# Kernel optimization log

Hardware: AMD Instinct MI355X
Metric: run time of the kernel (lower is better)

Reference implementation:

```python
import jax, jax.numpy as jnp
import numpy as np

N_NODES = 100000
N_EDGES = 1600000
DIM = 64
LAYERS = 2


def setup_inputs() -> dict:
    key = jax.random.key(0)
    k1, k2, k3, k4 = jax.random.split(key, 4)
    h = jax.random.normal(k1, (N_NODES, DIM), dtype=jnp.float32)
    w = jax.random.uniform(k2, (N_EDGES,), dtype=jnp.float32)
    src = jax.random.randint(k3, (N_EDGES,), 0, N_NODES, dtype=jnp.int32)
    dst = jax.random.randint(k4, (N_EDGES,), 0, N_NODES, dtype=jnp.int32)
    return {"h": h, "w": w, "src": src, "dst": dst}


def reference(h, w, src, dst):
    N = h.shape[0]
    # weighted in-degree, clamped at 1 (DGL in_degrees(weight='w').clamp(min=1))
    deg = jnp.maximum(jax.ops.segment_sum(w, dst, num_segments=N), 1.0)
    norm = deg[:, None] ** -0.5  # [N, 1]
    embs = [h]
    for _ in range(LAYERS):
        h_norm = h * norm                              # [N, d]
        m = h_norm[src] * w[:, None]                   # [E, d] edge messages (u_mul_e)
        neigh_sum = jax.ops.segment_sum(m, dst, num_segments=N)  # fn.sum
        h = neigh_sum * norm
        embs.append(h)
    # mean over [h0, h1, ..., hL]
    return jnp.mean(jnp.stack(embs, axis=1), axis=1)
```

## Files before the change

### kernel.cpp

```cpp
#include <hip/hip_runtime.h>
#include <hip/hip_bf16.h>

#define D 64
#define THREADS 256
#define BKT_BITS 9
#define BKT_NODES (1 << BKT_BITS)
#define CHUNK 8192

__device__ __forceinline__ unsigned f2bf(float f) {
    unsigned u = __float_as_uint(f);
    return (u + 0x7fffu + ((u >> 16) & 1u)) >> 16;
}
__device__ __forceinline__ float2 bfpair(unsigned v) {
    return make_float2(__uint_as_float(v << 16), __uint_as_float(v & 0xffff0000u));
}

typedef unsigned long long u64t;
typedef float f32x4 __attribute__((ext_vector_type(4)));
typedef unsigned u32x4 __attribute__((ext_vector_type(4)));

__device__ __forceinline__ int2 ldnt_int2(const int2* p) {
    u64t v = __builtin_nontemporal_load((const u64t*)p);
    int2 r;
    r.x = (int)(unsigned)(v & 0xffffffffull);
    r.y = (int)(unsigned)(v >> 32);
    return r;
}
__device__ __forceinline__ uint4 ldnt_uint4(const uint4* p) {
    u32x4 v = __builtin_nontemporal_load((const u32x4*)p);
    return make_uint4(v.x, v.y, v.z, v.w);
}
__device__ __forceinline__ void stnt_f4(float4 v, float4* p) {
    f32x4 t = {v.x, v.y, v.z, v.w};
    __builtin_nontemporal_store(t, (f32x4*)p);
}
__device__ __forceinline__ void stnt_u4(uint4 v, uint4* p) {
    u32x4 t = {v.x, v.y, v.z, v.w};
    __builtin_nontemporal_store(t, (u32x4*)p);
}

__global__ void p1a_hist(const int* __restrict__ dst, int* __restrict__ blockCount,
                         int E, int B) {
    __shared__ int lc[256];
    int t = threadIdx.x;
    lc[t] = 0;
    __syncthreads();
    int base = blockIdx.x * CHUNK;
    int end = min(base + CHUNK, E);
    int end4 = end >> 2;
    for (int e4 = (base >> 2) + t; e4 < end4; e4 += THREADS) {
        int4 d4 = ((const int4*)dst)[e4];
        atomicAdd(&lc[d4.x >> BKT_BITS], 1);
        atomicAdd(&lc[d4.y >> BKT_BITS], 1);
        atomicAdd(&lc[d4.z >> BKT_BITS], 1);
        atomicAdd(&lc[d4.w >> BKT_BITS], 1);
    }
    for (int e = (end4 << 2) + t; e < end; e += THREADS)
        atomicAdd(&lc[dst[e] >> BKT_BITS], 1);
    __syncthreads();
    if (t < B) blockCount[(long long)blockIdx.x * B + t] = lc[t];
}

__global__ void p1b_scanblocks(int* __restrict__ blockCount, int* __restrict__ total,
                               int NBLK, int B) {
    __shared__ int sm[256];
    int b = blockIdx.x, t = threadIdx.x;
    int run = 0;
    for (int base = 0; base < NBLK; base += 256) {
        int i = base + t;
        int v = (i < NBLK) ? blockCount[(long long)i * B + b] : 0;
        sm[t] = v;
        __syncthreads();
        for (int off = 1; off < 256; off <<= 1) {
            int u = (t >= off) ? sm[t - off] : 0;
            __syncthreads();
            sm[t] += u;
            __syncthreads();
        }
        if (i < NBLK) blockCount[(long long)i * B + b] = run + sm[t] - v;
        run += sm[255];
        __syncthreads();
    }
    if (t == 0) total[b] = run;
}

__global__ void p1c_scanbuckets(const int* __restrict__ total, int* __restrict__ bstart,
                                int B, int E) {
    __shared__ int sm[256];
    int t = threadIdx.x;
    int run = 0;
    for (int base = 0; base < B; base += 256) {
        int i = base + t;
        int v = (i < B) ? total[i] : 0;
        sm[t] = v;
        __syncthreads();
        for (int off = 1; off < 256; off <<= 1) {
            int u = (t >= off) ? sm[t - off] : 0;
            __syncthreads();
            sm[t] += u;
            __syncthreads();
        }
        if (i < B) bstart[i] = run + sm[t] - v;
        run += sm[255];
        __syncthreads();
    }
    if (t == 0) bstart[B] = E;
}

__global__ void p1d_scatter(const int* __restrict__ dst, const int* __restrict__ src,
                            const float* __restrict__ w, const int* __restrict__ blockCount,
                            const int* __restrict__ bstart, int2* __restrict__ temp,
                            int E, int B) {
    __shared__ int cur[256];
    int t = threadIdx.x;
    if (t < B) cur[t] = bstart[t] + blockCount[(long long)blockIdx.x * B + t];
    __syncthreads();
    int base = blockIdx.x * CHUNK;
    int end = min(base + CHUNK, E);
    int end4 = end >> 2;
    for (int e4 = (base >> 2) + t; e4 < end4; e4 += THREADS) {
        int4 d4 = ((const int4*)dst)[e4];
        int4 s4 = ((const int4*)src)[e4];
        float4 w4 = ((const float4*)w)[e4];
        int pos;
        pos = atomicAdd(&cur[d4.x >> BKT_BITS], 1);
        temp[pos] = make_int2(s4.x | ((d4.x & (BKT_NODES - 1)) << 17), __float_as_int(w4.x));
        pos = atomicAdd(&cur[d4.y >> BKT_BITS], 1);
        temp[pos] = make_int2(s4.y | ((d4.y & (BKT_NODES - 1)) << 17), __float_as_int(w4.y));
        pos = atomicAdd(&cur[d4.z >> BKT_BITS], 1);
        temp[pos] = make_int2(s4.z | ((d4.z & (BKT_NODES - 1)) << 17), __float_as_int(w4.z));
        pos = atomicAdd(&cur[d4.w >> BKT_BITS], 1);
        temp[pos] = make_int2(s4.w | ((d4.w & (BKT_NODES - 1)) << 17), __float_as_int(w4.w));
    }
    for (int e = (end4 << 2) + t; e < end; e += THREADS) {
        int d = dst[e];
        int pos = atomicAdd(&cur[d >> BKT_BITS], 1);
        temp[pos] = make_int2(src[e] | ((d & (BKT_NODES - 1)) << 17), __float_as_int(w[e]));
    }
}

__global__ void p2a_build(const int2* __restrict__ temp, const int* __restrict__ bstart,
                          int* __restrict__ rowptr, float* __restrict__ norm,
                          int N, int E, int B) {
    __shared__ int cnt[BKT_NODES];
    __shared__ float degs[BKT_NODES];
    __shared__ int sm[256];
    int b = blockIdx.x, t = threadIdx.x;
    int ebeg = bstart[b], eend = bstart[b + 1];
    for (int i = t; i < BKT_NODES; i += THREADS) { cnt[i] = 0; degs[i] = 0.0f; }
    __syncthreads();
    for (int e = ebeg + t; e < eend; e += THREADS) {
        int2 pk = temp[e];
        int dl = (pk.x >> 17) & (BKT_NODES - 1);
        atomicAdd(&cnt[dl], 1);
        atomicAdd(&degs[dl], __int_as_float(pk.y));
    }
    __syncthreads();
    int node0 = b << BKT_BITS;
    int run = 0;
    for (int base = 0; base < BKT_NODES; base += 256) {
        int v = cnt[base + t];
        sm[t] = v;
        __syncthreads();
        for (int off = 1; off < 256; off <<= 1) {
            int u = (t >= off) ? sm[t - off] : 0;
            __syncthreads();
            sm[t] += u;
            __syncthreads();
        }
        int node = node0 + base + t;
        if (node < N) {
            rowptr[node] = ebeg + run + sm[t] - v;
            norm[node] = rsqrtf(fmaxf(degs[base + t], 1.0f));
        }
        run += sm[255];
        __syncthreads();
    }
    if (b == 0 && t == 0) rowptr[N] = E;
}

__global__ void p2b_place(const int2* __restrict__ temp, const int* __restrict__ bstart,
                          const int* __restrict__ rowptr, const float* __restrict__ norm,
                          int2* __restrict__ packed, int N, int E) {
    __shared__ int cur[BKT_NODES];
    int b = blockIdx.x, t = threadIdx.x;
    int ebeg = bstart[b], eend = bstart[b + 1];
    int node0 = b << BKT_BITS;
    for (int i = t; i < BKT_NODES; i += THREADS) {
        int node = node0 + i;
        cur[i] = (node < N) ? (rowptr[node] - ebeg) : 0;
    }
    __syncthreads();
    for (int e = ebeg + t; e < eend; e += THREADS) {
        int2 pk = temp[e];
        int dl = (pk.x >> 17) & (BKT_NODES - 1);
        int s = pk.x & 0x1ffff;
        float coef = __int_as_float(pk.y) * norm[s];
        int pos = atomicAdd(&cur[dl], 1);
        packed[ebeg + pos] = make_int2(s, __float_as_int(coef));
    }
}

__global__ void tobf16_kernel(const float* __restrict__ h, unsigned* __restrict__ hbf2,
                              long long nd4) {
    long long i = (long long)blockIdx.x * blockDim.x + threadIdx.x;
    if (i < nd4) {
        float4 v = ((const float4*)h)[i];
        ((uint2*)hbf2)[i] = make_uint2(f2bf(v.x) | (f2bf(v.y) << 16),
                                       f2bf(v.z) | (f2bf(v.w) << 16));
    }
}

#define EDGE_FMA(r, c, A0, A1, A2, A3, A4, A5, A6, A7) do {            \
    float2 fa = bfpair((r).x), fb = bfpair((r).y);                      \
    float2 fc = bfpair((r).z), fd = bfpair((r).w);                      \
    A0 = fmaf(fa.x, (c), A0); A1 = fmaf(fa.y, (c), A1);                 \
    A2 = fmaf(fb.x, (c), A2); A3 = fmaf(fb.y, (c), A3);                 \
    A4 = fmaf(fc.x, (c), A4); A5 = fmaf(fc.y, (c), A5);                 \
    A6 = fmaf(fd.x, (c), A6); A7 = fmaf(fd.y, (c), A7); } while (0)

__global__ void gather1_kernel(const uint4* __restrict__ h_in, const int2* __restrict__ packed,
                               const int* __restrict__ rowptr, const float* __restrict__ norm,
                               uint4* __restrict__ h_out, int N) {
    int node = blockIdx.x * (blockDim.x >> 3) + (threadIdx.x >> 3);
    int lane = threadIdx.x & 7;
    if (node >= N) return;
    int j = rowptr[node], end = rowptr[node + 1];
    float a0 = 0, a1 = 0, a2 = 0, a3 = 0, a4 = 0, a5 = 0, a6 = 0, a7 = 0;
    float b0 = 0, b1 = 0, b2 = 0, b3 = 0, b4 = 0, b5 = 0, b6 = 0, b7 = 0;
    for (; j + 8 <= end; j += 8) {
        int2 p0 = ldnt_int2(&packed[j + 0]), p1 = ldnt_int2(&packed[j + 1]);
        int2 p2 = ldnt_int2(&packed[j + 2]), p3 = ldnt_int2(&packed[j + 3]);
        int2 p4 = ldnt_int2(&packed[j + 4]), p5 = ldnt_int2(&packed[j + 5]);
        int2 p6 = ldnt_int2(&packed[j + 6]), p7 = ldnt_int2(&packed[j + 7]);
        uint4 r0 = h_in[((long long)p0.x << 3) + lane];
        uint4 r1 = h_in[((long long)p1.x << 3) + lane];
        uint4 r2 = h_in[((long long)p2.x << 3) + lane];
        uint4 r3 = h_in[((long long)p3.x << 3) + lane];
        uint4 r4 = h_in[((long long)p4.x << 3) + lane];
        uint4 r5 = h_in[((long long)p5.x << 3) + lane];
        uint4 r6 = h_in[((long long)p6.x << 3) + lane];
        uint4 r7 = h_in[((long long)p7.x << 3) + lane];
        EDGE_FMA(r0, __int_as_float(p0.y), a0, a1, a2, a3, a4, a5, a6, a7);
        EDGE_FMA(r1, __int_as_float(p1.y), b0, b1, b2, b3, b4, b5, b6, b7);
        EDGE_FMA(r2, __int_as_float(p2.y), a0, a1, a2, a3, a4, a5, a6, a7);
        EDGE_FMA(r3, __int_as_float(p3.y), b0, b1, b2, b3, b4, b5, b6, b7);
        EDGE_FMA(r4, __int_as_float(p4.y), a0, a1, a2, a3, a4, a5, a6, a7);
        EDGE_FMA(r5, __int_as_float(p5.y), b0, b1, b2, b3, b4, b5, b6, b7);
        EDGE_FMA(r6, __int_as_float(p6.y), a0, a1, a2, a3, a4, a5, a6, a7);
        EDGE_FMA(r7, __int_as_float(p7.y), b0, b1, b2, b3, b4, b5, b6, b7);
    }
    for (; j + 4 <= end; j += 4) {
        int2 p0 = ldnt_int2(&packed[j + 0]), p1 = ldnt_int2(&packed[j + 1]);
        int2 p2 = ldnt_int2(&packed[j + 2]), p3 = ldnt_int2(&packed[j + 3]);
        uint4 r0 = h_in[((long long)p0.x << 3) + lane];
        uint4 r1 = h_in[((long long)p1.x << 3) + lane];
        uint4 r2 = h_in[((long long)p2.x << 3) + lane];
        uint4 r3 = h_in[((long long)p3.x << 3) + lane];
        EDGE_FMA(r0, __int_as_float(p0.y), a0, a1, a2, a3, a4, a5, a6, a7);
        EDGE_FMA(r1, __int_as_float(p1.y), b0, b1, b2, b3, b4, b5, b6, b7);
        EDGE_FMA(r2, __int_as_float(p2.y), a0, a1, a2, a3, a4, a5, a6, a7);
        EDGE_FMA(r3, __int_as_float(p3.y), b0, b1, b2, b3, b4, b5, b6, b7);
    }
    for (; j < end; ++j) {
        int2 p = ldnt_int2(&packed[j]);
        uint4 r = h_in[((long long)p.x << 3) + lane];
        EDGE_FMA(r, __int_as_float(p.y), a0, a1, a2, a3, a4, a5, a6, a7);
    }
    float nv = norm[node];
    float d0 = (a0 + b0) * nv, d1 = (a1 + b1) * nv, d2 = (a2 + b2) * nv, d3 = (a3 + b3) * nv;
    float d4 = (a4 + b4) * nv, d5 = (a5 + b5) * nv, d6 = (a6 + b6) * nv, d7 = (a7 + b7) * nv;
    stnt_u4(make_uint4(f2bf(d0) | (f2bf(d1) << 16), f2bf(d2) | (f2bf(d3) << 16),
                       f2bf(d4) | (f2bf(d5) << 16), f2bf(d6) | (f2bf(d7) << 16)),
            &h_out[((long long)node << 3) + lane]);
}

__global__ void gather2_final_kernel(const uint4* __restrict__ h0bf, const uint4* __restrict__ h1bf,
                                     const int2* __restrict__ packed, const int* __restrict__ rowptr,
                                     const float* __restrict__ norm, float* __restrict__ out, int N) {
    int node = blockIdx.x * (blockDim.x >> 3) + (threadIdx.x >> 3);
    int lane = threadIdx.x & 7;
    if (node >= N) return;
    int j = rowptr[node], end = rowptr[node + 1];
    float a0 = 0, a1 = 0, a2 = 0, a3 = 0, a4 = 0, a5 = 0, a6 = 0, a7 = 0;
    float b0 = 0, b1 = 0, b2 = 0, b3 = 0, b4 = 0, b5 = 0, b6 = 0, b7 = 0;
    for (; j + 8 <= end; j += 8) {
        int2 p0 = ldnt_int2(&packed[j + 0]), p1 = ldnt_int2(&packed[j + 1]);
        int2 p2 = ldnt_int2(&packed[j + 2]), p3 = ldnt_int2(&packed[j + 3]);
        int2 p4 = ldnt_int2(&packed[j + 4]), p5 = ldnt_int2(&packed[j + 5]);
        int2 p6 = ldnt_int2(&packed[j + 6]), p7 = ldnt_int2(&packed[j + 7]);
        uint4 r0 = h1bf[((long long)p0.x << 3) + lane];
        uint4 r1 = h1bf[((long long)p1.x << 3) + lane];
        uint4 r2 = h1bf[((long long)p2.x << 3) + lane];
        uint4 r3 = h1bf[((long long)p3.x << 3) + lane];
        uint4 r4 = h1bf[((long long)p4.x << 3) + lane];
        uint4 r5 = h1bf[((long long)p5.x << 3) + lane];
        uint4 r6 = h1bf[((long long)p6.x << 3) + lane];
        uint4 r7 = h1bf[((long long)p7.x << 3) + lane];
        EDGE_FMA(r0, __int_as_float(p0.y), a0, a1, a2, a3, a4, a5, a6, a7);
        EDGE_FMA(r1, __int_as_float(p1.y), b0, b1, b2, b3, b4, b5, b6, b7);
        EDGE_FMA(r2, __int_as_float(p2.y), a0, a1, a2, a3, a4, a5, a6, a7);
        EDGE_FMA(r3, __int_as_float(p3.y), b0, b1, b2, b3, b4, b5, b6, b7);
        EDGE_FMA(r4, __int_as_float(p4.y), a0, a1, a2, a3, a4, a5, a6, a7);
        EDGE_FMA(r5, __int_as_float(p5.y), b0, b1, b2, b3, b4, b5, b6, b7);
        EDGE_FMA(r6, __int_as_float(p6.y), a0, a1, a2, a3, a4, a5, a6, a7);
        EDGE_FMA(r7, __int_as_float(p7.y), b0, b1, b2, b3, b4, b5, b6, b7);
    }
    for (; j + 4 <= end; j += 4) {
        int2 p0 = ldnt_int2(&packed[j + 0]), p1 = ldnt_int2(&packed[j + 1]);
        int2 p2 = ldnt_int2(&packed[j + 2]), p3 = ldnt_int2(&packed[j + 3]);
        uint4 r0 = h1bf[((long long)p0.x << 3) + lane];
        uint4 r1 = h1bf[((long long)p1.x << 3) + lane];
        uint4 r2 = h1bf[((long long)p2.x << 3) + lane];
        uint4 r3 = h1bf[((long long)p3.x << 3) + lane];
        EDGE_FMA(r0, __int_as_float(p0.y), a0, a1, a2, a3, a4, a5, a6, a7);
        EDGE_FMA(r1, __int_as_float(p1.y), b0, b1, b2, b3, b4, b5, b6, b7);
        EDGE_FMA(r2, __int_as_float(p2.y), a0, a1, a2, a3, a4, a5, a6, a7);
        EDGE_FMA(r3, __int_as_float(p3.y), b0, b1, b2, b3, b4, b5, b6, b7);
    }
    for (; j < end; ++j) {
        int2 p = ldnt_int2(&packed[j]);
        uint4 r = h1bf[((long long)p.x << 3) + lane];
        EDGE_FMA(r, __int_as_float(p.y), a0, a1, a2, a3, a4, a5, a6, a7);
    }
    long long idx = ((long long)node << 3) + lane;
    float nv = norm[node];
    uint4 h0r = ldnt_uint4(&h0bf[idx]);
    uint4 h1r = h1bf[idx];
    float2 h0a = bfpair(h0r.x), h0b = bfpair(h0r.y), h0c = bfpair(h0r.z), h0d = bfpair(h0r.w);
    float2 h1a = bfpair(h1r.x), h1b = bfpair(h1r.y), h1c = bfpair(h1r.z), h1d = bfpair(h1r.w);
    float4 o0, o1;
    o0.x = (h0a.x + h1a.x + (a0 + b0) * nv) * (1.0f / 3.0f);
    o0.y = (h0a.y + h1a.y + (a1 + b1) * nv) * (1.0f / 3.0f);
    o0.z = (h0b.x + h1b.x + (a2 + b2) * nv) * (1.0f / 3.0f);
    o0.w = (h0b.y + h1b.y + (a3 + b3) * nv) * (1.0f / 3.0f);
    o1.x = (h0c.x + h1c.x + (a4 + b4) * nv) * (1.0f / 3.0f);
    o1.y = (h0c.y + h1c.y + (a5 + b5) * nv) * (1.0f / 3.0f);
    o1.z = (h0d.x + h1d.x + (a6 + b6) * nv) * (1.0f / 3.0f);
    o1.w = (h0d.y + h1d.y + (a7 + b7) * nv) * (1.0f / 3.0f);
    stnt_f4(o0, &((float4*)out)[((long long)node << 4) + (lane << 1)]);
    stnt_f4(o1, &((float4*)out)[((long long)node << 4) + (lane << 1) + 1]);
}

extern "C" void kernel_launch(void* const* d_in, const int* in_sizes, int n_in,
                              void* d_out, int out_size, void* d_ws, size_t ws_size,
                              hipStream_t stream) {
    const float* h   = (const float*)d_in[0];
    const float* w   = (const float*)d_in[1];
    const int*   src = (const int*)d_in[2];
    const int*   dst = (const int*)d_in[3];
    const int N = in_sizes[0] / D;
    const int E = in_sizes[1];
    float* out = (float*)d_out;

    const int B = (N + BKT_NODES - 1) >> BKT_BITS;
    const int NBLK = (E + CHUNK - 1) / CHUNK;

    char* ws = (char*)d_ws;
    size_t off = 0;
    auto alloc = [&](size_t bytes, size_t align) -> char* {
        off = (off + align - 1) & ~(align - 1);
        char* p = ws + off;
        off += bytes;
        return p;
    };
    float* norm     = (float*)alloc((size_t)N * 4, 16);
    int*   rowptr   = (int*)  alloc((size_t)(N + 1) * 4, 16);
    int*   total    = (int*)  alloc((size_t)B * 4, 16);
    int*   bstart   = (int*)  alloc((size_t)(B + 1) * 4, 16);
    int*   blockCnt = (int*)  alloc((size_t)NBLK * B * 4, 16);
    int2*  packed   = (int2*) alloc((size_t)E * 8, 128);
    char*  shared_region = alloc((size_t)E * 8, 128);
    int2*     temp = (int2*)shared_region;
    unsigned* h1bf = (unsigned*)shared_region;
    unsigned* h0bf = (unsigned*)alloc((size_t)N * D * 2, 128);

    const int nodes_per_block = THREADS / 8;
    const int gather_blocks = (N + nodes_per_block - 1) / nodes_per_block;
    const long long nd4 = (long long)N * D / 4;
    const int cvt_blocks = (int)((nd4 + THREADS - 1) / THREADS);

    p1a_hist<<<NBLK, THREADS, 0, stream>>>(dst, blockCnt, E, B);
    p1b_scanblocks<<<B, 256, 0, stream>>>(blockCnt, total, NBLK, B);
    p1c_scanbuckets<<<1, 256, 0, stream>>>(total, bstart, B, E);
    p1d_scatter<<<NBLK, THREADS, 0, stream>>>(dst, src, w, blockCnt, bstart, temp, E, B);
    p2a_build<<<B, 256, 0, stream>>>(temp, bstart, rowptr, norm, N, E, B);
    p2b_place<<<B, 256, 0, stream>>>(temp, bstart, rowptr, norm, packed, N, E);

    tobf16_kernel<<<cvt_blocks, THREADS, 0, stream>>>(h, h0bf, nd4);

    gather1_kernel<<<gather_blocks, THREADS, 0, stream>>>((const uint4*)h0bf, packed, rowptr,
                                                          norm, (uint4*)h1bf, N);
    gather2_final_kernel<<<gather_blocks, THREADS, 0, stream>>>((const uint4*)h0bf, (const uint4*)h1bf,
                                                                packed, rowptr, norm, out, N);
}
```

Baseline: 223.4 us.

## Fuse CSR build kernels, fold bf16 cast into histogram, apply source norm in gather

Merges p2a_build and p2b_place into one kernel that keeps the per-node cursors in shared memory, so packed edges are placed without a rowptr round trip or an extra launch. The fp32-to-bf16 conversion of h moves into the histogram kernel as a grid-stride loop, and CHUNK is halved so that kernel launches more blocks. Source-node normalisation now happens in the gather kernels, each edge loading norm[src] instead of using a precomputed coefficient. Nontemporal loads are replaced with plain loads. The cost is an extra random 4-byte norm load per edge, read twice across the two gather passes.

```diff
diff --git a/kernel.cpp b/kernel.cpp
--- a/kernel.cpp
+++ b/kernel.cpp
@@ -5,7 +5,7 @@
 #define THREADS 256
 #define BKT_BITS 9
 #define BKT_NODES (1 << BKT_BITS)
-#define CHUNK 8192
+#define CHUNK 4096
 
 __device__ __forceinline__ unsigned f2bf(float f) {
     unsigned u = __float_as_uint(f);
@@ -15,21 +15,8 @@
     return make_float2(__uint_as_float(v << 16), __uint_as_float(v & 0xffff0000u));
 }
 
-typedef unsigned long long u64t;
 typedef float f32x4 __attribute__((ext_vector_type(4)));
 typedef unsigned u32x4 __attribute__((ext_vector_type(4)));
-
-__device__ __forceinline__ int2 ldnt_int2(const int2* p) {
-    u64t v = __builtin_nontemporal_load((const u64t*)p);
-    int2 r;
-    r.x = (int)(unsigned)(v & 0xffffffffull);
-    r.y = (int)(unsigned)(v >> 32);
-    return r;
-}
-__device__ __forceinline__ uint4 ldnt_uint4(const uint4* p) {
-    u32x4 v = __builtin_nontemporal_load((const u32x4*)p);
-    return make_uint4(v.x, v.y, v.z, v.w);
-}
 __device__ __forceinline__ void stnt_f4(float4 v, float4* p) {
     f32x4 t = {v.x, v.y, v.z, v.w};
     __builtin_nontemporal_store(t, (f32x4*)p);
@@ -40,11 +27,18 @@
 }
 
 __global__ void p1a_hist(const int* __restrict__ dst, int* __restrict__ blockCount,
-                         int E, int B) {
+                         const float* __restrict__ h, unsigned* __restrict__ hbf2,
+                         long long nd4, int E, int B) {
     __shared__ int lc[256];
     int t = threadIdx.x;
     lc[t] = 0;
     __syncthreads();
+    for (long long i = (long long)blockIdx.x * THREADS + t; i < nd4;
+         i += (long long)gridDim.x * THREADS) {
+        float4 v = ((const float4*)h)[i];
+        ((uint2*)hbf2)[i] = make_uint2(f2bf(v.x) | (f2bf(v.y) << 16),
+                                       f2bf(v.z) | (f2bf(v.w) << 16));
+    }
     int base = blockIdx.x * CHUNK;
     int end = min(base + CHUNK, E);
     int end4 = end >> 2;
@@ -139,11 +133,12 @@
     }
 }
 
-__global__ void p2a_build(const int2* __restrict__ temp, const int* __restrict__ bstart,
-                          int* __restrict__ rowptr, float* __restrict__ norm,
-                          int N, int E, int B) {
+__global__ void p2_build(const int2* __restrict__ temp, const int* __restrict__ bstart,
+                         int2* __restrict__ packed, int* __restrict__ rowptr,
+                         float* __restrict__ norm, int N, int E, int B) {
     __shared__ int cnt[BKT_NODES];
     __shared__ float degs[BKT_NODES];
+    __shared__ int cur[BKT_NODES];
     __shared__ int sm[256];
     int b = blockIdx.x, t = threadIdx.x;
     int ebeg = bstart[b], eend = bstart[b + 1];
@@ -156,7 +151,6 @@
         atomicAdd(&degs[dl], __int_as_float(pk.y));
     }
     __syncthreads();
-    int node0 = b << BKT_BITS;
     int run = 0;
     for (int base = 0; base < BKT_NODES; base += 256) {
         int v = cnt[base + t];
@@ -168,46 +162,25 @@
             sm[t] += u;
             __syncthreads();
         }
-        int node = node0 + base + t;
-        if (node < N) {
-            rowptr[node] = ebeg + run + sm[t] - v;
-            norm[node] = rsqrtf(fmaxf(degs[base + t], 1.0f));
-        }
+        cur[base + t] = run + sm[t] - v;
         run += sm[255];
         __syncthreads();
     }
-    if (b == 0 && t == 0) rowptr[N] = E;
-}
-
-__global__ void p2b_place(const int2* __restrict__ temp, const int* __restrict__ bstart,
-                          const int* __restrict__ rowptr, const float* __restrict__ norm,
-                          int2* __restrict__ packed, int N, int E) {
-    __shared__ int cur[BKT_NODES];
-    int b = blockIdx.x, t = threadIdx.x;
-    int ebeg = bstart[b], eend = bstart[b + 1];
     int node0 = b << BKT_BITS;
     for (int i = t; i < BKT_NODES; i += THREADS) {
         int node = node0 + i;
-        cur[i] = (node < N) ? (rowptr[node] - ebeg) : 0;
-    }
+        if (node < N) {
+            rowptr[node] = ebeg + cur[i];
+            norm[node] = rsqrtf(fmaxf(degs[i], 1.0f));
+        }
+    }
+    if (b == 0 && t == 0) rowptr[N] = E;
     __syncthreads();
     for (int e = ebeg + t; e < eend; e += THREADS) {
         int2 pk = temp[e];
         int dl = (pk.x >> 17) & (BKT_NODES - 1);
-        int s = pk.x & 0x1ffff;
-        float coef = __int_as_float(pk.y) * norm[s];
         int pos = atomicAdd(&cur[dl], 1);
-        packed[ebeg + pos] = make_int2(s, __float_as_int(coef));
-    }
-}
-
-__global__ void tobf16_kernel(const float* __restrict__ h, unsigned* __restrict__ hbf2,
-                              long long nd4) {
-    long long i = (long long)blockIdx.x * blockDim.x + threadIdx.x;
-    if (i < nd4) {
-        float4 v = ((const float4*)h)[i];
-        ((uint2*)hbf2)[i] = make_uint2(f2bf(v.x) | (f2bf(v.y) << 16),
-                                       f2bf(v.z) | (f2bf(v.w) << 16));
+        packed[ebeg + pos] = make_int2(pk.x & 0x1ffff, pk.y);
     }
 }
 
@@ -229,10 +202,8 @@
     float a0 = 0, a1 = 0, a2 = 0, a3 = 0, a4 = 0, a5 = 0, a6 = 0, a7 = 0;
     float b0 = 0, b1 = 0, b2 = 0, b3 = 0, b4 = 0, b5 = 0, b6 = 0, b7 = 0;
     for (; j + 8 <= end; j += 8) {
-        int2 p0 = ldnt_int2(&packed[j + 0]), p1 = ldnt_int2(&packed[j + 1]);
-        int2 p2 = ldnt_int2(&packed[j + 2]), p3 = ldnt_int2(&packed[j + 3]);
-        int2 p4 = ldnt_int2(&packed[j + 4]), p5 = ldnt_int2(&packed[j + 5]);
-        int2 p6 = ldnt_int2(&packed[j + 6]), p7 = ldnt_int2(&packed[j + 7]);
+        int2 p0 = packed[j + 0], p1 = packed[j + 1], p2 = packed[j + 2], p3 = packed[j + 3];
+        int2 p4 = packed[j + 4], p5 = packed[j + 5], p6 = packed[j + 6], p7 = packed[j + 7];
         uint4 r0 = h_in[((long long)p0.x << 3) + lane];
         uint4 r1 = h_in[((long long)p1.x << 3) + lane];
         uint4 r2 = h_in[((long long)p2.x << 3) + lane];
@@ -241,31 +212,43 @@
         uint4 r5 = h_in[((long long)p5.x << 3) + lane];
         uint4 r6 = h_in[((long long)p6.x << 3) + lane];
         uint4 r7 = h_in[((long long)p7.x << 3) + lane];
-        EDGE_FMA(r0, __int_as_float(p0.y), a0, a1, a2, a3, a4, a5, a6, a7);
-        EDGE_FMA(r1, __int_as_float(p1.y), b0, b1, b2, b3, b4, b5, b6, b7);
-        EDGE_FMA(r2, __int_as_float(p2.y), a0, a1, a2, a3, a4, a5, a6, a7);
-        EDGE_FMA(r3, __int_as_float(p3.y), b0, b1, b2, b3, b4, b5, b6, b7);
-        EDGE_FMA(r4, __int_as_float(p4.y), a0, a1, a2, a3, a4, a5, a6, a7);
-        EDGE_FMA(r5, __int_as_float(p5.y), b0, b1, b2, b3, b4, b5, b6, b7);
-        EDGE_FMA(r6, __int_as_float(p6.y), a0, a1, a2, a3, a4, a5, a6, a7);
-        EDGE_FMA(r7, __int_as_float(p7.y), b0, b1, b2, b3, b4, b5, b6, b7);
+        float c0 = __int_as_float(p0.y) * norm[p0.x];
+        float c1 = __int_as_float(p1.y) * norm[p1.x];
+        float c2 = __int_as_float(p2.y) * norm[p2.x];
+        float c3 = __int_as_float(p3.y) * norm[p3.x];
+        float c4 = __int_as_float(p4.y) * norm[p4.x];
+        float c5 = __int_as_float(p5.y) * norm[p5.x];
+        float c6 = __int_as_float(p6.y) * norm[p6.x];
+        float c7 = __int_as_float(p7.y) * norm[p7.x];
+        EDGE_FMA(r0, c0, a0, a1, a2, a3, a4, a5, a6, a7);
+        EDGE_FMA(r1, c1, b0, b1, b2, b3, b4, b5, b6, b7);
+        EDGE_FMA(r2, c2, a0, a1, a2, a3, a4, a5, a6, a7);
+        EDGE_FMA(r3, c3, b0, b1, b2, b3, b4, b5, b6, b7);
+        EDGE_FMA(r4, c4, a0, a1, a2, a3, a4, a5, a6, a7);
+        EDGE_FMA(r5, c5, b0, b1, b2, b3, b4, b5, b6, b7);
+        EDGE_FMA(r6, c6, a0, a1, a2, a3, a4, a5, a6, a7);
+        EDGE_FMA(r7, c7, b0, b1, b2, b3, b4, b5, b6, b7);
     }
     for (; j + 4 <= end; j += 4) {
-        int2 p0 = ldnt_int2(&packed[j + 0]), p1 = ldnt_int2(&packed[j + 1]);
-        int2 p2 = ldnt_int2(&packed[j + 2]), p3 = ldnt_int2(&packed[j + 3]);
+        int2 p0 = packed[j + 0], p1 = packed[j + 1], p2 = packed[j + 2], p3 = packed[j + 3];
         uint4 r0 = h_in[((long long)p0.x << 3) + lane];
         uint4 r1 = h_in[((long long)p1.x << 3) + lane];
         uint4 r2 = h_in[((long long)p2.x << 3) + lane];
         uint4 r3 = h_in[((long long)p3.x << 3) + lane];
-        EDGE_FMA(r0, __int_as_float(p0.y), a0, a1, a2, a3, a4, a5, a6, a7);
-        EDGE_FMA(r1, __int_as_float(p1.y), b0, b1, b2, b3, b4, b5, b6, b7);
-        EDGE_FMA(r2, __int_as_float(p2.y), a0, a1, a2, a3, a4, a5, a6, a7);
-        EDGE_FMA(r3, __int_as_float(p3.y), b0, b1, b2, b3, b4, b5, b6, b7);
+        float c0 = __int_as_float(p0.y) * norm[p0.x];
+        float c1 = __int_as_float(p1.y) * norm[p1.x];
+        float c2 = __int_as_float(p2.y) * norm[p2.x];
+        float c3 = __int_as_float(p3.y) * norm[p3.x];
+        EDGE_FMA(r0, c0, a0, a1, a2, a3, a4, a5, a6, a7);
+        EDGE_FMA(r1, c1, b0, b1, b2, b3, b4, b5, b6, b7);
+        EDGE_FMA(r2, c2, a0, a1, a2, a3, a4, a5, a6, a7);
+        EDGE_FMA(r3, c3, b0, b1, b2, b3, b4, b5, b6, b7);
     }
     for (; j < end; ++j) {
-        int2 p = ldnt_int2(&packed[j]);
+        int2 p = packed[j];
         uint4 r = h_in[((long long)p.x << 3) + lane];
-        EDGE_FMA(r, __int_as_float(p.y), a0, a1, a2, a3, a4, a5, a6, a7);
+        float c = __int_as_float(p.y) * norm[p.x];
+        EDGE_FMA(r, c, a0, a1, a2, a3, a4, a5, a6, a7);
     }
     float nv = norm[node];
     float d0 = (a0 + b0) * nv, d1 = (a1 + b1) * nv, d2 = (a2 + b2) * nv, d3 = (a3 + b3) * nv;
@@ -285,10 +268,8 @@
     float a0 = 0, a1 = 0, a2 = 0, a3 = 0, a4 = 0, a5 = 0, a6 = 0, a7 = 0;
     float b0 = 0, b1 = 0, b2 = 0, b3 = 0, b4 = 0, b5 = 0, b6 = 0, b7 = 0;
     for (; j + 8 <= end; j += 8) {
-        int2 p0 = ldnt_int2(&packed[j + 0]), p1 = ldnt_int2(&packed[j + 1]);
-        int2 p2 = ldnt_int2(&packed[j + 2]), p3 = ldnt_int2(&packed[j + 3]);
-        int2 p4 = ldnt_int2(&packed[j + 4]), p5 = ldnt_int2(&packed[j + 5]);
-        int2 p6 = ldnt_int2(&packed[j + 6]), p7 = ldnt_int2(&packed[j + 7]);
+        int2 p0 = packed[j + 0], p1 = packed[j + 1], p2 = packed[j + 2], p3 = packed[j + 3];
+        int2 p4 = packed[j + 4], p5 = packed[j + 5], p6 = packed[j + 6], p7 = packed[j + 7];
         uint4 r0 = h1bf[((long long)p0.x << 3) + lane];
         uint4 r1 = h1bf[((long long)p1.x << 3) + lane];
         uint4 r2 = h1bf[((long long)p2.x << 3) + lane];
@@ -297,35 +278,47 @@
         uint4 r5 = h1bf[((long long)p5.x << 3) + lane];
         uint4 r6 = h1bf[((long long)p6.x << 3) + lane];
         uint4 r7 = h1bf[((long long)p7.x << 3) + lane];
-        EDGE_FMA(r0, __int_as_float(p0.y), a0, a1, a2, a3, a4, a5, a6, a7);
-        EDGE_FMA(r1, __int_as_float(p1.y), b0, b1, b2, b3, b4, b5, b6, b7);
-        EDGE_FMA(r2, __int_as_float(p2.y), a0, a1, a2, a3, a4, a5, a6, a7);
-        EDGE_FMA(r3, __int_as_float(p3.y), b0, b1, b2, b3, b4, b5, b6, b7);
-        EDGE_FMA(r4, __int_as_float(p4.y), a0, a1, a2, a3, a4, a5, a6, a7);
-        EDGE_FMA(r5, __int_as_float(p5.y), b0, b1, b2, b3, b4, b5, b6, b7);
-        EDGE_FMA(r6, __int_as_float(p6.y), a0, a1, a2, a3, a4, a5, a6, a7);
-        EDGE_FMA(r7, __int_as_float(p7.y), b0, b1, b2, b3, b4, b5, b6, b7);
+        float c0 = __int_as_float(p0.y) * norm[p0.x];
+        float c1 = __int_as_float(p1.y) * norm[p1.x];
+        float c2 = __int_as_float(p2.y) * norm[p2.x];
+        float c3 = __int_as_float(p3.y) * norm[p3.x];
+        float c4 = __int_as_float(p4.y) * norm[p4.x];
+        float c5 = __int_as_float(p5.y) * norm[p5.x];
+        float c6 = __int_as_float(p6.y) * norm[p6.x];
+        float c7 = __int_as_float(p7.y) * norm[p7.x];
+        EDGE_FMA(r0, c0, a0, a1, a2, a3, a4, a5, a6, a7);
+        EDGE_FMA(r1, c1, b0, b1, b2, b3, b4, b5, b6, b7);
+        EDGE_FMA(r2, c2, a0, a1, a2, a3, a4, a5, a6, a7);
+        EDGE_FMA(r3, c3, b0, b1, b2, b3, b4, b5, b6, b7);
+        EDGE_FMA(r4, c4, a0, a1, a2, a3, a4, a5, a6, a7);
+        EDGE_FMA(r5, c5, b0, b1, b2, b3, b4, b5, b6, b7);
+        EDGE_FMA(r6, c6, a0, a1, a2, a3, a4, a5, a6, a7);
+        EDGE_FMA(r7, c7, b0, b1, b2, b3, b4, b5, b6, b7);
     }
     for (; j + 4 <= end; j += 4) {
-        int2 p0 = ldnt_int2(&packed[j + 0]), p1 = ldnt_int2(&packed[j + 1]);
-        int2 p2 = ldnt_int2(&packed[j + 2]), p3 = ldnt_int2(&packed[j + 3]);
+        int2 p0 = packed[j + 0], p1 = packed[j + 1], p2 = packed[j + 2], p3 = packed[j + 3];
         uint4 r0 = h1bf[((long long)p0.x << 3) + lane];
         uint4 r1 = h1bf[((long long)p1.x << 3) + lane];
         uint4 r2 = h1bf[((long long)p2.x << 3) + lane];
         uint4 r3 = h1bf[((long long)p3.x << 3) + lane];
-        EDGE_FMA(r0, __int_as_float(p0.y), a0, a1, a2, a3, a4, a5, a6, a7);
-        EDGE_FMA(r1, __int_as_float(p1.y), b0, b1, b2, b3, b4, b5, b6, b7);
-        EDGE_FMA(r2, __int_as_float(p2.y), a0, a1, a2, a3, a4, a5, a6, a7);
-        EDGE_FMA(r3, __int_as_float(p3.y), b0, b1, b2, b3, b4, b5, b6, b7);
+        float c0 = __int_as_float(p0.y) * norm[p0.x];
+        float c1 = __int_as_float(p1.y) * norm[p1.x];
+        float c2 = __int_as_float(p2.y) * norm[p2.x];
+        float c3 = __int_as_float(p3.y) * norm[p3.x];
+        EDGE_FMA(r0, c0, a0, a1, a2, a3, a4, a5, a6, a7);
+        EDGE_FMA(r1, c1, b0, b1, b2, b3, b4, b5, b6, b7);
+        EDGE_FMA(r2, c2, a0, a1, a2, a3, a4, a5, a6, a7);
+        EDGE_FMA(r3, c3, b0, b1, b2, b3, b4, b5, b6, b7);
     }
     for (; j < end; ++j) {
-        int2 p = ldnt_int2(&packed[j]);
+        int2 p = packed[j];
         uint4 r = h1bf[((long long)p.x << 3) + lane];
-        EDGE_FMA(r, __int_as_float(p.y), a0, a1, a2, a3, a4, a5, a6, a7);
+        float c = __int_as_float(p.y) * norm[p.x];
+        EDGE_FMA(r, c, a0, a1, a2, a3, a4, a5, a6, a7);
     }
     long long idx = ((long long)node << 3) + lane;
     float nv = norm[node];
-    uint4 h0r = ldnt_uint4(&h0bf[idx]);
+    uint4 h0r = h0bf[idx];
     uint4 h1r = h1bf[idx];
     float2 h0a = bfpair(h0r.x), h0b = bfpair(h0r.y), h0c = bfpair(h0r.z), h0d = bfpair(h0r.w);
     float2 h1a = bfpair(h1r.x), h1b = bfpair(h1r.y), h1c = bfpair(h1r.z), h1d = bfpair(h1r.w);
@@ -378,16 +371,12 @@
     const int nodes_per_block = THREADS / 8;
     const int gather_blocks = (N + nodes_per_block - 1) / nodes_per_block;
     const long long nd4 = (long long)N * D / 4;
-    const int cvt_blocks = (int)((nd4 + THREADS - 1) / THREADS);
-
-    p1a_hist<<<NBLK, THREADS, 0, stream>>>(dst, blockCnt, E, B);
+
+    p1a_hist<<<NBLK, THREADS, 0, stream>>>(dst, blockCnt, h, h0bf, nd4, E, B);
     p1b_scanblocks<<<B, 256, 0, stream>>>(blockCnt, total, NBLK, B);
     p1c_scanbuckets<<<1, 256, 0, stream>>>(total, bstart, B, E);
     p1d_scatter<<<NBLK, THREADS, 0, stream>>>(dst, src, w, blockCnt, bstart, temp, E, B);
-    p2a_build<<<B, 256, 0, stream>>>(temp, bstart, rowptr, norm, N, E, B);
-    p2b_place<<<B, 256, 0, stream>>>(temp, bstart, rowptr, norm, packed, N, E);
-
-    tobf16_kernel<<<cvt_blocks, THREADS, 0, stream>>>(h, h0bf, nd4);
+    p2_build<<<B, 256, 0, stream>>>(temp, bstart, packed, rowptr, norm, N, E, B);
 
     gather1_kernel<<<gather_blocks, THREADS, 0, stream>>>((const uint4*)h0bf, packed, rowptr,
                                                           norm, (uint4*)h1bf, N);
```

Result: no change. 220.0 us (-1.5%).
